# Performance work log

Hardware: AMD Instinct MI355X
Metric: run time of the kernel (lower is better)

## Reference

```python
import jax, jax.numpy as jnp
import numpy as np

# token_type_vocab constants (closed over; original passes a dict)
WORD_TOKEN, SMILES_TOKEN, VALUE_TOKEN, CLS_TOKEN, SEP_TOKEN, MASK_TOKEN = 0, 1, 2, 3, 4, 5
FP_DIM, HID, COL_VOCAB, MAX_POS, TT_VOCAB = 768, 768, 1000, 512, 8
B, S = 64, 512


def setup_inputs() -> dict:
    key = jax.random.key(0)
    ks = jax.random.split(key, 16)
    scale = 0.02
    return {
        "batch_size": B,
        "max_batch_seq_len": S,
        "SMILES_fps": jax.random.normal(ks[0], (B, S, FP_DIM), jnp.float32),
        "word_tokens_ref": jax.random.randint(ks[1], (B, S), 0, COL_VOCAB),
        "values_ref": jax.random.normal(ks[2], (B, S), jnp.float32),
        "token_type_ids": jax.random.randint(ks[3], (B, S), 0, 6),
        "position_ids": jax.random.randint(ks[4], (B, S), 0, MAX_POS),
        "fc1_w": jax.random.normal(ks[5], (FP_DIM, 4 * FP_DIM), jnp.float32) * scale,
        "fc1_b": jnp.zeros((4 * FP_DIM,), jnp.float32),
        "fc2_w": jax.random.normal(ks[6], (4 * FP_DIM, HID), jnp.float32) * scale,
        "fc2_b": jnp.zeros((HID,), jnp.float32),
        "prop_emb": jax.random.normal(ks[7], (COL_VOCAB, HID), jnp.float32) * scale,
        "val_w": jax.random.normal(ks[8], (HID,), jnp.float32) * scale,  # Linear(1, HID) weight
        "val_b": jnp.zeros((HID,), jnp.float32),
        "pos_emb": jax.random.normal(ks[9], (MAX_POS, HID), jnp.float32) * scale,
        "type_emb": jax.random.normal(ks[10], (TT_VOCAB, HID), jnp.float32) * scale,
        "ln_g": jnp.ones((HID,), jnp.float32),
        "ln_b": jnp.zeros((HID,), jnp.float32),
    }


def reference(batch_size, max_batch_seq_len, SMILES_fps, word_tokens_ref, values_ref,
              token_type_ids, position_ids, fc1_w, fc1_b, fc2_w, fc2_b, prop_emb,
              val_w, val_b, pos_emb, type_emb, ln_g, ln_b):
    word_mask = token_type_ids == WORD_TOKEN
    smiles_mask = token_type_ids == SMILES_TOKEN
    value_mask = token_type_ids == VALUE_TOKEN
    # Faithful to source: '&' of mutually exclusive equalities -> always False
    special_mask = (token_type_ids == CLS_TOKEN) & (token_type_ids == SEP_TOKEN) & (token_type_ids == MASK_TOKEN)

    # branch embeddings computed densely, selected per token (masks are disjoint)
    word_e = prop_emb[word_tokens_ref]                                   # [B,S,H]
    smiles_e = jax.nn.relu(jnp.einsum('bsf,fd->bsd', SMILES_fps, fc1_w) + fc1_b)
    smiles_e = jnp.einsum('bsf,fd->bsd', smiles_e, fc2_w) + fc2_b        # [B,S,H]
    value_e = values_ref[..., None] * val_w + val_b                      # [B,S,H]
    special_e = type_emb[token_type_ids]                                 # [B,S,H]

    input_embeddings = jnp.zeros_like(word_e)
    input_embeddings = jnp.where(word_mask[..., None], word_e, input_embeddings)
    input_embeddings = jnp.where(smiles_mask[..., None], smiles_e, input_embeddings)
    input_embeddings = jnp.where(value_mask[..., None], value_e, input_embeddings)
    input_embeddings = jnp.where(special_mask[..., None], special_e, input_embeddings)

    emb = input_embeddings + pos_emb[position_ids] + type_emb[token_type_ids]
    mu = jnp.mean(emb, axis=-1, keepdims=True)
    var = jnp.mean(jnp.square(emb - mu), axis=-1, keepdims=True)
    emb = (emb - mu) * jax.lax.rsqrt(var + 1e-12) * ln_g + ln_b
    return emb  # dropout_rate=0 (eval): identity
```

## Files before the change

### kernel.cpp

```cpp
#include <hip/hip_runtime.h>
#include <hip/hip_bf16.h>
#include <stdint.h>


typedef __bf16 bf16x8 __attribute__((ext_vector_type(8)));
typedef float f32x4 __attribute__((ext_vector_type(4)));

__device__ __forceinline__ unsigned short f2bf(float f) {
  union { float f; unsigned int u; } c; c.f = f;
  unsigned int u = c.u;
  return (unsigned short)((u + 0x7FFFu + ((u >> 16) & 1u)) >> 16);
}
__device__ __forceinline__ float bf2f(unsigned short b) {
  union { unsigned int u; float f; } c; c.u = ((unsigned int)b) << 16;
  return c.f;
}
__device__ __forceinline__ unsigned pk2(float a, float b) {
  return (unsigned)f2bf(a) | ((unsigned)f2bf(b) << 16);
}
__device__ __forceinline__ void barrier_sync() {
  asm volatile("" ::: "memory");
  __builtin_amdgcn_sched_barrier(0);
  __builtin_amdgcn_s_barrier();
  __builtin_amdgcn_sched_barrier(0);
  asm volatile("" ::: "memory");
}

__global__ __launch_bounds__(256) void k_prep(
    const float* __restrict__ fc1_w, const float* __restrict__ fc2_w,
    unsigned short* __restrict__ w1t, unsigned short* __restrict__ w2t,
    int* __restrict__ counter) {
  if (blockIdx.x == 0 && threadIdx.x == 0) *counter = 0;
  __shared__ float tile[32][33];
  int b = blockIdx.x;
  const float* src;
  unsigned short* dst;
  int R, C, bx, by;
  if (b < 2304) {
    src = fc1_w; dst = w1t; R = 768; C = 3072;
    bx = (b % 96) * 32; by = (b / 96) * 32;
  } else {
    b -= 2304;
    src = fc2_w; dst = w2t; R = 3072; C = 768;
    bx = (b % 24) * 32; by = (b / 24) * 32;
  }
  int tx = threadIdx.x & 31;
  int ty = threadIdx.x >> 5;
#pragma unroll
  for (int i = 0; i < 4; i++) {
    int r = by + ty + i * 8;
    tile[ty + i * 8][tx] = src[(size_t)r * C + bx + tx];
  }
  __syncthreads();
#pragma unroll
  for (int i = 0; i < 4; i++) {
    int c = bx + ty + i * 8;
    dst[(size_t)c * R + by + tx] = f2bf(tile[tx][ty + i * 8]);
  }
}

__global__ void k_compact(const int* __restrict__ tt, int* __restrict__ counter,
                          int* __restrict__ idx, int* __restrict__ slot, int BS) {
  int t = blockIdx.x * 256 + threadIdx.x;
  if (t >= BS) return;
  if (tt[t] == 1) {
    int s = atomicAdd(counter, 1);
    idx[s] = t;
    slot[t] = s;
  }
}

__global__ __launch_bounds__(256) void k_gemm1(
    const float* __restrict__ fps, const int* __restrict__ idx,
    const unsigned short* __restrict__ BT,
    const float* __restrict__ bias,
    unsigned short* __restrict__ C,
    const int* __restrict__ counter, int cap) {
  int n = *counter;
  int n_pad = (n + 127) & ~127;
  if (n_pad > cap) n_pad = cap;
  const int mb = n_pad >> 7;

  const int bid = blockIdx.x;
  const int xcd = bid & 7;
  const int j = bid >> 3;
  const int mc = xcd >> 1, cc = xcd & 1;
  const int q = mb >> 2, r = mb & 3;
  const int mlen = q + (mc < r ? 1 : 0);
  const int mbase = mc * q + (mc < r ? mc : r);
  if (j >= mlen * 12) return;
  const int m_blk = mbase + j / 12;
  const int nb = cc * 12 + j % 12;
  const int m0 = m_blk * 128, n0 = nb * 128;

  __shared__ __attribute__((aligned(128))) char smem[65536];
  auto lds = (__attribute__((address_space(3))) char*)smem;
  const int t = threadIdx.x;
  const int wave = t >> 6, lane = t & 63;
  const int wm = (wave >> 1) * 64, wn = (wave & 1) * 64;

  const float* arow[4];
  bool avalid[4];
#pragma unroll
  for (int i = 0; i < 4; i++) {
    int c = i * 256 + t;
    int rr = c >> 3;
    int koff = ((c & 7) ^ (rr & 7)) << 3;
    int grow = m0 + rr;
    avalid[i] = grow < n;
    arow[i] = fps + (size_t)(avalid[i] ? idx[grow] : 0) * 768 + koff;
  }

  f32x4 acc[4][4] = {};
  float4 av[4][2];

  auto loadA = [&](int kt) {
#pragma unroll
    for (int i = 0; i < 4; i++) {
      if (avalid[i]) {
        const float4* p = (const float4*)(arow[i] + kt * 64);
        av[i][0] = p[0];
        av[i][1] = p[1];
      } else {
        av[i][0] = make_float4(0.f, 0.f, 0.f, 0.f);
        av[i][1] = make_float4(0.f, 0.f, 0.f, 0.f);
      }
    }
  };
  auto stageB = [&](int kt, int bufbase) {
#pragma unroll
    for (int i = 0; i < 4; i++) {
      int c = i * 256 + t;
      int rr = c >> 3;
      const unsigned short* gb =
          BT + (size_t)(n0 + rr) * 768 + kt * 64 + (((c & 7) ^ (rr & 7)) << 3);
      __builtin_amdgcn_global_load_lds(
          (const __attribute__((address_space(1))) void*)gb,
          (__attribute__((address_space(3))) void*)(lds + bufbase + 16384 +
                                                    i * 4096 + wave * 1024),
          16, 0, 0);
    }
  };
  auto writeA = [&](int bufbase) {
#pragma unroll
    for (int i = 0; i < 4; i++) {
      int c = i * 256 + t;
      uint4 w;
      w.x = pk2(av[i][0].x, av[i][0].y);
      w.y = pk2(av[i][0].z, av[i][0].w);
      w.z = pk2(av[i][1].x, av[i][1].y);
      w.w = pk2(av[i][1].z, av[i][1].w);
      *(uint4*)(smem + bufbase + c * 16) = w;
    }
  };
  auto compute = [&](int bufbase) {
#pragma unroll
    for (int kk = 0; kk < 2; kk++) {
      bf16x8 af[4], bfr[4];
      int kbyte = (kk * 32 + ((lane >> 4) * 8)) * 2;
#pragma unroll
      for (int mi = 0; mi < 4; mi++) {
        int rr = wm + mi * 16 + (lane & 15);
        af[mi] = *(const bf16x8*)(smem + bufbase + rr * 128 + (kbyte ^ ((rr & 7) << 4)));
      }
#pragma unroll
      for (int ni = 0; ni < 4; ni++) {
        int rr = wn + ni * 16 + (lane & 15);
        bfr[ni] = *(const bf16x8*)(smem + bufbase + 16384 + rr * 128 + (kbyte ^ ((rr & 7) << 4)));
      }
#pragma unroll
      for (int mi = 0; mi < 4; mi++)
#pragma unroll
        for (int ni = 0; ni < 4; ni++)
          acc[mi][ni] = __builtin_amdgcn_mfma_f32_16x16x32_bf16(
              af[mi], bfr[ni], acc[mi][ni], 0, 0, 0);
    }
  };

  loadA(0);
  stageB(0, 0);
  writeA(0);
  asm volatile("s_waitcnt lgkmcnt(0)" ::: "memory");

  for (int it = 0; it < 12; ++it) {
    const int cur = it & 1, nxt = cur ^ 1;
    if (it + 1 < 12) {
      loadA(it + 1);
      stageB(it + 1, nxt * 32768);
      __builtin_amdgcn_sched_barrier(0);
      asm volatile("s_waitcnt vmcnt(12)" ::: "memory");
    } else {
      asm volatile("s_waitcnt vmcnt(0)" ::: "memory");
    }
    barrier_sync();
    compute(cur * 32768);
    if (it + 1 < 12) writeA(nxt * 32768);
    asm volatile("s_waitcnt lgkmcnt(0)" ::: "memory");
    barrier_sync();
  }

#pragma unroll
  for (int ni = 0; ni < 4; ni++) {
    int col = n0 + wn + ni * 16 + (lane & 15);
    float bv = bias[col];
#pragma unroll
    for (int mi = 0; mi < 4; mi++) {
#pragma unroll
      for (int j2 = 0; j2 < 4; j2++) {
        int row = m0 + wm + mi * 16 + ((lane >> 4) * 4) + j2;
        float v = acc[mi][ni][j2] + bv;
        v = v > 0.f ? v : 0.f;
        C[(size_t)row * 3072 + col] = f2bf(v);
      }
    }
  }
}

template <int NB, int KS>
__global__ __launch_bounds__(256) void k_gemm2(
    const unsigned short* __restrict__ A,
    const unsigned short* __restrict__ BT,
    unsigned short* __restrict__ C,
    const int* __restrict__ counter, int cap) {
  int n = *counter;
  int n_pad = (n + 127) & ~127;
  if (n_pad > cap) n_pad = cap;
  const int mb = n_pad >> 7;

  constexpr int NCOL = NB * KS;
  constexpr int C_CH = (KS == 4) ? 4 : 2;
  constexpr int A_CH = 8 / C_CH;
  constexpr int CLEN = NCOL / C_CH;

  const int bid = blockIdx.x;
  const int xcd = bid & 7;
  const int j = bid >> 3;
  const int mc = xcd / C_CH, cc = xcd % C_CH;
  const int q = mb / A_CH, r = mb % A_CH;
  const int mlen = q + (mc < r ? 1 : 0);
  const int mbase = mc * q + (mc < r ? mc : r);
  if (j >= mlen * CLEN) return;
  const int m_blk = mbase + j / CLEN;
  const int c_blk = cc * CLEN + j % CLEN;
  const int ks = c_blk / NB;
  const int nb = c_blk % NB;
  const int m0 = m_blk * 128, n0 = nb * 128;
  const int k0g = ks * 768;

  __shared__ __attribute__((aligned(128))) char smem[65536];
  auto lds = (__attribute__((address_space(3))) char*)smem;
  const int t = threadIdx.x;
  const int wave = t >> 6, lane = t & 63;
  const int wm = (wave >> 1) * 64, wn = (wave & 1) * 64;

  f32x4 acc[4][4] = {};

  auto stage = [&](int kt, int bufbase) {
#pragma unroll
    for (int i = 0; i < 4; i++) {
      int c = i * 256 + t;
      int rr = c >> 3;
      int k8 = ((c & 7) ^ (rr & 7)) << 3;
      const unsigned short* ga = A + (size_t)(m0 + rr) * 3072 + k0g + kt * 64 + k8;
      __builtin_amdgcn_global_load_lds(
          (const __attribute__((address_space(1))) void*)ga,
          (__attribute__((address_space(3))) void*)(lds + bufbase + i * 4096 + wave * 1024),
          16, 0, 0);
    }
#pragma unroll
    for (int i = 0; i < 4; i++) {
      int c = i * 256 + t;
      int rr = c >> 3;
      int k8 = ((c & 7) ^ (rr & 7)) << 3;
      const unsigned short* gb = BT + (size_t)(n0 + rr) * 3072 + k0g + kt * 64 + k8;
      __builtin_amdgcn_global_load_lds(
          (const __attribute__((address_space(1))) void*)gb,
          (__attribute__((address_space(3))) void*)(lds + bufbase + 16384 + i * 4096 + wave * 1024),
          16, 0, 0);
    }
  };

  stage(0, 0);
  for (int it = 0; it < 12; ++it) {
    const int cur = it & 1, nxt = cur ^ 1;
    if (it + 1 < 12) {
      stage(it + 1, nxt * 32768);
      __builtin_amdgcn_sched_barrier(0);
      asm volatile("s_waitcnt vmcnt(8)" ::: "memory");
    } else {
      asm volatile("s_waitcnt vmcnt(0)" ::: "memory");
    }
    barrier_sync();
#pragma unroll
    for (int kk = 0; kk < 2; kk++) {
      bf16x8 af[4], bfr[4];
      int kbyte = (kk * 32 + ((lane >> 4) * 8)) * 2;
      const int bufbase = cur * 32768;
#pragma unroll
      for (int mi = 0; mi < 4; mi++) {
        int rr = wm + mi * 16 + (lane & 15);
        af[mi] = *(const bf16x8*)(smem + bufbase + rr * 128 + (kbyte ^ ((rr & 7) << 4)));
      }
#pragma unroll
      for (int ni = 0; ni < 4; ni++) {
        int rr = wn + ni * 16 + (lane & 15);
        bfr[ni] = *(const bf16x8*)(smem + bufbase + 16384 + rr * 128 + (kbyte ^ ((rr & 7) << 4)));
      }
#pragma unroll
      for (int mi = 0; mi < 4; mi++)
#pragma unroll
        for (int ni = 0; ni < 4; ni++)
          acc[mi][ni] = __builtin_amdgcn_mfma_f32_16x16x32_bf16(
              af[mi], bfr[ni], acc[mi][ni], 0, 0, 0);
    }
    asm volatile("s_waitcnt lgkmcnt(0)" ::: "memory");
    barrier_sync();
  }

#pragma unroll
  for (int ni = 0; ni < 4; ni++) {
    int col = n0 + wn + ni * 16 + (lane & 15);
#pragma unroll
    for (int mi = 0; mi < 4; mi++) {
#pragma unroll
      for (int j2 = 0; j2 < 4; j2++) {
        int row = m0 + wm + mi * 16 + ((lane >> 4) * 4) + j2;
        C[((size_t)ks * cap + row) * 768 + col] = f2bf(acc[mi][ni][j2]);
      }
    }
  }
}

template <int KS>
__global__ __launch_bounds__(256) void k_assemble(
    const unsigned short* __restrict__ sout, const float* __restrict__ fc2b,
    const int* __restrict__ slot,
    const int* __restrict__ ttid, const int* __restrict__ word,
    const float* __restrict__ values, const int* __restrict__ posid,
    const float* __restrict__ prop, const float* __restrict__ valw,
    const float* __restrict__ valb, const float* __restrict__ pose,
    const float* __restrict__ tye, const float* __restrict__ lng,
    const float* __restrict__ lnb, float* __restrict__ out, int BS, int cap) {
  int wave = threadIdx.x >> 6, lane = threadIdx.x & 63;
  int t = blockIdx.x * 4 + wave;
  if (t >= BS) return;
  int tt = ttid[t];

  float v[12];
  if (tt == 1) {
    int sl = slot[t];
    const ushort4* pr[KS];
#pragma unroll
    for (int p = 0; p < KS; p++)
      pr[p] = (const ushort4*)(sout + ((size_t)p * cap + sl) * 768);
    const float4* b4 = (const float4*)fc2b;
#pragma unroll
    for (int i = 0; i < 3; i++) {
      float4 b = b4[lane + (i << 6)];
      float a0 = b.x, a1 = b.y, a2 = b.z, a3 = b.w;
#pragma unroll
      for (int p = 0; p < KS; p++) {
        ushort4 u = pr[p][lane + (i << 6)];
        a0 += bf2f(u.x); a1 += bf2f(u.y); a2 += bf2f(u.z); a3 += bf2f(u.w);
      }
      v[4 * i] = a0; v[4 * i + 1] = a1; v[4 * i + 2] = a2; v[4 * i + 3] = a3;
    }
  } else if (tt == 0) {
    const float4* row = (const float4*)(prop + (size_t)word[t] * 768);
#pragma unroll
    for (int i = 0; i < 3; i++) {
      float4 x = row[lane + (i << 6)];
      v[4 * i] = x.x; v[4 * i + 1] = x.y; v[4 * i + 2] = x.z; v[4 * i + 3] = x.w;
    }
  } else if (tt == 2) {
    float val = values[t];
#pragma unroll
    for (int i = 0; i < 3; i++) {
      float4 w = ((const float4*)valw)[lane + (i << 6)];
      float4 b = ((const float4*)valb)[lane + (i << 6)];
      v[4 * i] = val * w.x + b.x; v[4 * i + 1] = val * w.y + b.y;
      v[4 * i + 2] = val * w.z + b.z; v[4 * i + 3] = val * w.w + b.w;
    }
  } else {
#pragma unroll
    for (int j = 0; j < 12; j++) v[j] = 0.f;
  }

  const float4* p4 = (const float4*)(pose + (size_t)posid[t] * 768);
  const float4* ty4 = (const float4*)(tye + (size_t)tt * 768);
#pragma unroll
  for (int i = 0; i < 3; i++) {
    float4 p = p4[lane + (i << 6)];
    float4 y = ty4[lane + (i << 6)];
    v[4 * i] += p.x + y.x; v[4 * i + 1] += p.y + y.y;
    v[4 * i + 2] += p.z + y.z; v[4 * i + 3] += p.w + y.w;
  }

  float s = 0.f;
#pragma unroll
  for (int j = 0; j < 12; j++) s += v[j];
#pragma unroll
  for (int o = 32; o >= 1; o >>= 1) s += __shfl_xor(s, o);
  float mu = s * (1.0f / 768.0f);

  float qv = 0.f;
#pragma unroll
  for (int j = 0; j < 12; j++) { float d = v[j] - mu; qv += d * d; }
#pragma unroll
  for (int o = 32; o >= 1; o >>= 1) qv += __shfl_xor(qv, o);
  float rs = 1.0f / sqrtf(qv * (1.0f / 768.0f) + 1e-12f);

  float4* o4 = (float4*)(out + (size_t)t * 768);
#pragma unroll
  for (int i = 0; i < 3; i++) {
    float4 g = ((const float4*)lng)[lane + (i << 6)];
    float4 b = ((const float4*)lnb)[lane + (i << 6)];
    float4 r;
    r.x = (v[4 * i] - mu) * rs * g.x + b.x;
    r.y = (v[4 * i + 1] - mu) * rs * g.y + b.y;
    r.z = (v[4 * i + 2] - mu) * rs * g.z + b.z;
    r.w = (v[4 * i + 3] - mu) * rs * g.w + b.w;
    o4[lane + (i << 6)] = r;
  }
}

extern "C" void kernel_launch(void* const* d_in, const int* in_sizes, int n_in,
                              void* d_out, int out_size, void* d_ws, size_t ws_size,
                              hipStream_t stream) {
  const int BS = in_sizes[3];
  const float* fps    = (const float*)d_in[2];
  const int*   word   = (const int*)d_in[3];
  const float* values = (const float*)d_in[4];
  const int*   tt     = (const int*)d_in[5];
  const int*   pos    = (const int*)d_in[6];
  const float* fc1_w  = (const float*)d_in[7];
  const float* fc1_b  = (const float*)d_in[8];
  const float* fc2_w  = (const float*)d_in[9];
  const float* fc2_b  = (const float*)d_in[10];
  const float* prop   = (const float*)d_in[11];
  const float* valw   = (const float*)d_in[12];
  const float* valb   = (const float*)d_in[13];
  const float* pose   = (const float*)d_in[14];
  const float* tye    = (const float*)d_in[15];
  const float* lng    = (const float*)d_in[16];
  const float* lnb    = (const float*)d_in[17];
  float* out = (float*)d_out;

  char* ws = (char*)d_ws;
  const size_t off_idx  = 256;
  const size_t off_slot = off_idx + (size_t)BS * 4;
  const size_t off_w1t  = off_slot + (size_t)BS * 4;
  const size_t off_w2t  = off_w1t + (size_t)768 * 3072 * 2;
  const size_t off_h1   = off_w2t + (size_t)3072 * 768 * 2;
  const size_t fixed    = off_h1;
  size_t avail = ws_size > fixed ? ws_size - fixed : 0;

  const size_t per_tok4 = 3072 * 2 + 4 * 768 * 2;
  const bool splitk = avail >= (size_t)8192 * per_tok4;

  int cap;
  if (splitk) {
    cap = 8192;
  } else {
    const size_t per_tok1 = 3072 * 2 + 768 * 2;
    long c = (long)(avail / per_tok1);
    c &= ~511L;
    if (c > BS) c = BS;
    if (c < 512) c = 512;
    cap = (int)c;
  }
  const int MBcap = cap / 128;

  const size_t off_sout = off_h1 + (size_t)cap * 3072 * 2;

  int* counter = (int*)(ws + 0);
  int* idx     = (int*)(ws + off_idx);
  int* slot    = (int*)(ws + off_slot);
  unsigned short* w1t = (unsigned short*)(ws + off_w1t);
  unsigned short* w2t = (unsigned short*)(ws + off_w2t);
  unsigned short* h1  = (unsigned short*)(ws + off_h1);
  unsigned short* sout = (unsigned short*)(ws + off_sout);

  k_prep<<<4608, 256, 0, stream>>>(fc1_w, fc2_w, w1t, w2t, counter);
  k_compact<<<(BS + 255) / 256, 256, 0, stream>>>(tt, counter, idx, slot, BS);

  k_gemm1<<<24 * MBcap, 256, 0, stream>>>(fps, idx, w1t, fc1_b, h1, counter, cap);

  if (splitk) {
    k_gemm2<6, 4><<<24 * MBcap, 256, 0, stream>>>(h1, w2t, sout, counter, cap);
    k_assemble<4><<<(BS + 3) / 4, 256, 0, stream>>>(
        sout, fc2_b, slot, tt, word, values, pos, prop, valw, valb, pose, tye,
        lng, lnb, out, BS, cap);
  } else {
    k_gemm2<6, 1><<<6 * MBcap, 256, 0, stream>>>(h1, w2t, sout, counter, cap);
    k_assemble<1><<<(BS + 3) / 4, 256, 0, stream>>>(
        sout, fc2_b, slot, tt, word, values, pos, prop, valw, valb, pose, tye,
        lng, lnb, out, BS, cap);
  }
}
```

Before: 139.0 us.

## Pre-gather bf16 SMILES rows and overlap non-SMILES assembly with GEMM2

Gathers and converts the selected SMILES fp rows to bf16 in a separate pass fused into the weight-transpose kernel. GEMM1 can then stage both operands with direct global-to-LDS loads instead of register loads and in-kernel conversion. Non-SMILES token assembly and LayerNorm now run as extra blocks inside the GEMM2 launch, and a smaller kernel finalises only the SMILES tokens. This removes the slot array and trades an extra bf16 activation buffer and an extra pass over the gathered rows for a shorter GEMM1 inner loop and overlap of independent work.

```diff
diff --git a/kernel.cpp b/kernel.cpp
--- a/kernel.cpp
+++ b/kernel.cpp
@@ -14,9 +14,6 @@
 __device__ __forceinline__ float bf2f(unsigned short b) {
   union { unsigned int u; float f; } c; c.u = ((unsigned int)b) << 16;
   return c.f;
-}
-__device__ __forceinline__ unsigned pk2(float a, float b) {
-  return (unsigned)f2bf(a) | ((unsigned)f2bf(b) << 16);
 }
 __device__ __forceinline__ void barrier_sync() {
   asm volatile("" ::: "memory");
@@ -26,13 +23,77 @@
   asm volatile("" ::: "memory");
 }
 
-__global__ __launch_bounds__(256) void k_prep(
+__device__ __forceinline__ void ln_store(float v[12], const float* __restrict__ lng,
+                                         const float* __restrict__ lnb,
+                                         float* __restrict__ out, int t, int lane) {
+  float s = 0.f;
+#pragma unroll
+  for (int j = 0; j < 12; j++) s += v[j];
+#pragma unroll
+  for (int o = 32; o >= 1; o >>= 1) s += __shfl_xor(s, o);
+  float mu = s * (1.0f / 768.0f);
+  float qv = 0.f;
+#pragma unroll
+  for (int j = 0; j < 12; j++) { float d = v[j] - mu; qv += d * d; }
+#pragma unroll
+  for (int o = 32; o >= 1; o >>= 1) qv += __shfl_xor(qv, o);
+  float rs = 1.0f / sqrtf(qv * (1.0f / 768.0f) + 1e-12f);
+  float4* o4 = (float4*)(out + (size_t)t * 768);
+#pragma unroll
+  for (int i = 0; i < 3; i++) {
+    float4 g = ((const float4*)lng)[lane + (i << 6)];
+    float4 b = ((const float4*)lnb)[lane + (i << 6)];
+    float4 r;
+    r.x = (v[4 * i] - mu) * rs * g.x + b.x;
+    r.y = (v[4 * i + 1] - mu) * rs * g.y + b.y;
+    r.z = (v[4 * i + 2] - mu) * rs * g.z + b.z;
+    r.w = (v[4 * i + 3] - mu) * rs * g.w + b.w;
+    o4[lane + (i << 6)] = r;
+  }
+}
+
+__global__ void k_compact(const int* __restrict__ tt, int* __restrict__ counter,
+                          int* __restrict__ idx, int BS) {
+  int t = blockIdx.x * 256 + threadIdx.x;
+  if (t >= BS) return;
+  if (tt[t] == 1) {
+    int s = atomicAdd(counter, 1);
+    idx[s] = t;
+  }
+}
+
+__global__ __launch_bounds__(256) void k_prepg(
     const float* __restrict__ fc1_w, const float* __restrict__ fc2_w,
+    const float* __restrict__ fps, const int* __restrict__ idx,
+    const int* __restrict__ counter,
     unsigned short* __restrict__ w1t, unsigned short* __restrict__ w2t,
-    int* __restrict__ counter) {
-  if (blockIdx.x == 0 && threadIdx.x == 0) *counter = 0;
+    unsigned short* __restrict__ A1, int cap) {
+  int b = blockIdx.x;
+  if (b >= 4608) {
+    int wave = threadIdx.x >> 6, lane = threadIdx.x & 63;
+    int s = (b - 4608) * 4 + wave;
+    int n = *counter;
+    int n_pad = (n + 127) & ~127;
+    if (n_pad > cap) n_pad = cap;
+    if (s >= n_pad) return;
+    ushort4* dst = (ushort4*)(A1 + (size_t)s * 768);
+    if (s < n) {
+      const float4* srcr = (const float4*)(fps + (size_t)idx[s] * 768);
+#pragma unroll
+      for (int i = 0; i < 3; i++) {
+        float4 v = srcr[lane + (i << 6)];
+        ushort4 o;
+        o.x = f2bf(v.x); o.y = f2bf(v.y); o.z = f2bf(v.z); o.w = f2bf(v.w);
+        dst[lane + (i << 6)] = o;
+      }
+    } else {
+      ushort4 z = {0, 0, 0, 0};
+#pragma unroll
+      for (int i = 0; i < 3; i++) dst[lane + (i << 6)] = z;
+    }
+    return;
+  }
   __shared__ float tile[32][33];
-  int b = blockIdx.x;
   const float* src;
   unsigned short* dst;
   int R, C, bx, by;
@@ -59,22 +120,9 @@
   }
 }
 
-__global__ void k_compact(const int* __restrict__ tt, int* __restrict__ counter,
-                          int* __restrict__ idx, int* __restrict__ slot, int BS) {
-  int t = blockIdx.x * 256 + threadIdx.x;
-  if (t >= BS) return;
-  if (tt[t] == 1) {
-    int s = atomicAdd(counter, 1);
-    idx[s] = t;
-    slot[t] = s;
-  }
-}
-
 __global__ __launch_bounds__(256) void k_gemm1(
-    const float* __restrict__ fps, const int* __restrict__ idx,
-    const unsigned short* __restrict__ BT,
-    const float* __restrict__ bias,
-    unsigned short* __restrict__ C,
+    const unsigned short* __restrict__ A, const unsigned short* __restrict__ BT,
+    const float* __restrict__ bias, unsigned short* __restrict__ C,
     const int* __restrict__ counter, int cap) {
   int n = *counter;
   int n_pad = (n + 127) & ~127;
@@ -89,9 +137,8 @@
   const int mlen = q + (mc < r ? 1 : 0);
   const int mbase = mc * q + (mc < r ? mc : r);
   if (j >= mlen * 12) return;
-  const int m_blk = mbase + j / 12;
-  const int nb = cc * 12 + j % 12;
-  const int m0 = m_blk * 128, n0 = nb * 128;
+  const int m0 = (mbase + j / 12) * 128;
+  const int n0 = (cc * 12 + j % 12) * 128;
 
   __shared__ __attribute__((aligned(128))) char smem[65536];
   auto lds = (__attribute__((address_space(3))) char*)smem;
@@ -99,61 +146,45 @@
   const int wave = t >> 6, lane = t & 63;
   const int wm = (wave >> 1) * 64, wn = (wave & 1) * 64;
 
-  const float* arow[4];
-  bool avalid[4];
-#pragma unroll
-  for (int i = 0; i < 4; i++) {
-    int c = i * 256 + t;
-    int rr = c >> 3;
-    int koff = ((c & 7) ^ (rr & 7)) << 3;
-    int grow = m0 + rr;
-    avalid[i] = grow < n;
-    arow[i] = fps + (size_t)(avalid[i] ? idx[grow] : 0) * 768 + koff;
-  }
-
   f32x4 acc[4][4] = {};
-  float4 av[4][2];
-
-  auto loadA = [&](int kt) {
-#pragma unroll
-    for (int i = 0; i < 4; i++) {
-      if (avalid[i]) {
-        const float4* p = (const float4*)(arow[i] + kt * 64);
-        av[i][0] = p[0];
-        av[i][1] = p[1];
-      } else {
-        av[i][0] = make_float4(0.f, 0.f, 0.f, 0.f);
-        av[i][1] = make_float4(0.f, 0.f, 0.f, 0.f);
-      }
-    }
-  };
-  auto stageB = [&](int kt, int bufbase) {
+
+  auto stage = [&](int kt, int bufbase) {
 #pragma unroll
     for (int i = 0; i < 4; i++) {
       int c = i * 256 + t;
       int rr = c >> 3;
-      const unsigned short* gb =
-          BT + (size_t)(n0 + rr) * 768 + kt * 64 + (((c & 7) ^ (rr & 7)) << 3);
+      int k8 = ((c & 7) ^ (rr & 7)) << 3;
+      const unsigned short* ga = A + (size_t)(m0 + rr) * 768 + kt * 64 + k8;
+      __builtin_amdgcn_global_load_lds(
+          (const __attribute__((address_space(1))) void*)ga,
+          (__attribute__((address_space(3))) void*)(lds + bufbase + i * 4096 + wave * 1024),
+          16, 0, 0);
+    }
+#pragma unroll
+    for (int i = 0; i < 4; i++) {
+      int c = i * 256 + t;
+      int rr = c >> 3;
+      int k8 = ((c & 7) ^ (rr & 7)) << 3;
+      const unsigned short* gb = BT + (size_t)(n0 + rr) * 768 + kt * 64 + k8;
       __builtin_amdgcn_global_load_lds(
           (const __attribute__((address_space(1))) void*)gb,
-          (__attribute__((address_space(3))) void*)(lds + bufbase + 16384 +
-                                                    i * 4096 + wave * 1024),
+          (__attribute__((address_space(3))) void*)(lds + bufbase + 16384 + i * 4096 + wave * 1024),
           16, 0, 0);
     }
   };
-  auto writeA = [&](int bufbase) {
-#pragma unroll
-    for (int i = 0; i < 4; i++) {
-      int c = i * 256 + t;
-      uint4 w;
-      w.x = pk2(av[i][0].x, av[i][0].y);
-      w.y = pk2(av[i][0].z, av[i][0].w);
-      w.z = pk2(av[i][1].x, av[i][1].y);
-      w.w = pk2(av[i][1].z, av[i][1].w);
-      *(uint4*)(smem + bufbase + c * 16) = w;
-    }
-  };
-  auto compute = [&](int bufbase) {
+
+  stage(0, 0);
+  for (int it = 0; it < 12; ++it) {
+    const int cur = it & 1, nxt = cur ^ 1;
+    if (it + 1 < 12) {
+      stage(it + 1, nxt * 32768);
+      __builtin_amdgcn_sched_barrier(0);
+      asm volatile("s_waitcnt vmcnt(8)" ::: "memory");
+    } else {
+      asm volatile("s_waitcnt vmcnt(0)" ::: "memory");
+    }
+    barrier_sync();
+    const int bufbase = cur * 32768;
 #pragma unroll
     for (int kk = 0; kk < 2; kk++) {
       bf16x8 af[4], bfr[4];
@@ -175,26 +206,6 @@
           acc[mi][ni] = __builtin_amdgcn_mfma_f32_16x16x32_bf16(
               af[mi], bfr[ni], acc[mi][ni], 0, 0, 0);
     }
-  };
-
-  loadA(0);
-  stageB(0, 0);
-  writeA(0);
-  asm volatile("s_waitcnt lgkmcnt(0)" ::: "memory");
-
-  for (int it = 0; it < 12; ++it) {
-    const int cur = it & 1, nxt = cur ^ 1;
-    if (it + 1 < 12) {
-      loadA(it + 1);
-      stageB(it + 1, nxt * 32768);
-      __builtin_amdgcn_sched_barrier(0);
-      asm volatile("s_waitcnt vmcnt(12)" ::: "memory");
-    } else {
-      asm volatile("s_waitcnt vmcnt(0)" ::: "memory");
-    }
-    barrier_sync();
-    compute(cur * 32768);
-    if (it + 1 < 12) writeA(nxt * 32768);
     asm volatile("s_waitcnt lgkmcnt(0)" ::: "memory");
     barrier_sync();
   }
@@ -216,41 +227,82 @@
   }
 }
 
-template <int NB, int KS>
-__global__ __launch_bounds__(256) void k_gemm2(
+__global__ __launch_bounds__(256) void k_gemm2f(
     const unsigned short* __restrict__ A,
     const unsigned short* __restrict__ BT,
     unsigned short* __restrict__ C,
-    const int* __restrict__ counter, int cap) {
+    const int* __restrict__ counter, int cap, int NGEMM, int NASM,
+    const int* __restrict__ ttid, const int* __restrict__ word,
+    const float* __restrict__ values, const int* __restrict__ posid,
+    const float* __restrict__ prop, const float* __restrict__ valw,
+    const float* __restrict__ valb, const float* __restrict__ pose,
+    const float* __restrict__ tye, const float* __restrict__ lng,
+    const float* __restrict__ lnb, float* __restrict__ out, int BS) {
+  const int bid = blockIdx.x;
+  const int t = threadIdx.x;
+  const int wave = t >> 6, lane = t & 63;
+
+  if (bid >= NGEMM) {
+    int ab = bid - NGEMM;
+    for (int tok = ab * 4 + wave; tok < BS; tok += NASM * 4) {
+      int tt = ttid[tok];
+      if (tt == 1) continue;
+      float v[12];
+      if (tt == 0) {
+        const float4* row = (const float4*)(prop + (size_t)word[tok] * 768);
+#pragma unroll
+        for (int i = 0; i < 3; i++) {
+          float4 x = row[lane + (i << 6)];
+          v[4 * i] = x.x; v[4 * i + 1] = x.y; v[4 * i + 2] = x.z; v[4 * i + 3] = x.w;
+        }
+      } else if (tt == 2) {
+        float val = values[tok];
+#pragma unroll
+        for (int i = 0; i < 3; i++) {
+          float4 w = ((const float4*)valw)[lane + (i << 6)];
+          float4 b = ((const float4*)valb)[lane + (i << 6)];
+          v[4 * i] = val * w.x + b.x; v[4 * i + 1] = val * w.y + b.y;
+          v[4 * i + 2] = val * w.z + b.z; v[4 * i + 3] = val * w.w + b.w;
+        }
+      } else {
+#pragma unroll
+        for (int j = 0; j < 12; j++) v[j] = 0.f;
+      }
+      const float4* p4 = (const float4*)(pose + (size_t)posid[tok] * 768);
+      const float4* ty4 = (const float4*)(tye + (size_t)tt * 768);
+#pragma unroll
+      for (int i = 0; i < 3; i++) {
+        float4 p = p4[lane + (i << 6)];
+        float4 y = ty4[lane + (i << 6)];
+        v[4 * i] += p.x + y.x; v[4 * i + 1] += p.y + y.y;
+        v[4 * i + 2] += p.z + y.z; v[4 * i + 3] += p.w + y.w;
+      }
+      ln_store(v, lng, lnb, out, tok, lane);
+    }
+    return;
+  }
+
   int n = *counter;
   int n_pad = (n + 127) & ~127;
   if (n_pad > cap) n_pad = cap;
   const int mb = n_pad >> 7;
 
-  constexpr int NCOL = NB * KS;
-  constexpr int C_CH = (KS == 4) ? 4 : 2;
-  constexpr int A_CH = 8 / C_CH;
-  constexpr int CLEN = NCOL / C_CH;
-
-  const int bid = blockIdx.x;
   const int xcd = bid & 7;
   const int j = bid >> 3;
-  const int mc = xcd / C_CH, cc = xcd % C_CH;
-  const int q = mb / A_CH, r = mb % A_CH;
+  const int mc = xcd >> 2, cc = xcd & 3;
+  const int q = mb >> 1, r = mb & 1;
   const int mlen = q + (mc < r ? 1 : 0);
   const int mbase = mc * q + (mc < r ? mc : r);
-  if (j >= mlen * CLEN) return;
-  const int m_blk = mbase + j / CLEN;
-  const int c_blk = cc * CLEN + j % CLEN;
-  const int ks = c_blk / NB;
-  const int nb = c_blk % NB;
+  if (j >= mlen * 6) return;
+  const int m_blk = mbase + j / 6;
+  const int c_blk = cc * 6 + j % 6;
+  const int ks = c_blk / 6;
+  const int nb = c_blk % 6;
   const int m0 = m_blk * 128, n0 = nb * 128;
   const int k0g = ks * 768;
 
   __shared__ __attribute__((aligned(128))) char smem[65536];
   auto lds = (__attribute__((address_space(3))) char*)smem;
-  const int t = threadIdx.x;
-  const int wave = t >> 6, lane = t & 63;
   const int wm = (wave >> 1) * 64, wn = (wave & 1) * 64;
 
   f32x4 acc[4][4] = {};
@@ -291,11 +343,11 @@
       asm volatile("s_waitcnt vmcnt(0)" ::: "memory");
     }
     barrier_sync();
+    const int bufbase = cur * 32768;
 #pragma unroll
     for (int kk = 0; kk < 2; kk++) {
       bf16x8 af[4], bfr[4];
       int kbyte = (kk * 32 + ((lane >> 4) * 8)) * 2;
-      const int bufbase = cur * 32768;
 #pragma unroll
       for (int mi = 0; mi < 4; mi++) {
         int rr = wm + mi * 16 + (lane & 15);
@@ -331,63 +383,38 @@
   }
 }
 
-template <int KS>
-__global__ __launch_bounds__(256) void k_assemble(
+__global__ __launch_bounds__(256) void k_asm_s(
     const unsigned short* __restrict__ sout, const float* __restrict__ fc2b,
-    const int* __restrict__ slot,
-    const int* __restrict__ ttid, const int* __restrict__ word,
-    const float* __restrict__ values, const int* __restrict__ posid,
-    const float* __restrict__ prop, const float* __restrict__ valw,
-    const float* __restrict__ valb, const float* __restrict__ pose,
+    const int* __restrict__ idx, const int* __restrict__ counter,
+    const int* __restrict__ posid, const float* __restrict__ pose,
     const float* __restrict__ tye, const float* __restrict__ lng,
-    const float* __restrict__ lnb, float* __restrict__ out, int BS, int cap) {
+    const float* __restrict__ lnb, float* __restrict__ out, int cap) {
   int wave = threadIdx.x >> 6, lane = threadIdx.x & 63;
-  int t = blockIdx.x * 4 + wave;
-  if (t >= BS) return;
-  int tt = ttid[t];
+  int s = blockIdx.x * 4 + wave;
+  int n = *counter;
+  if (n > cap) n = cap;
+  if (s >= n) return;
+  int tok = idx[s];
 
   float v[12];
-  if (tt == 1) {
-    int sl = slot[t];
-    const ushort4* pr[KS];
-#pragma unroll
-    for (int p = 0; p < KS; p++)
-      pr[p] = (const ushort4*)(sout + ((size_t)p * cap + sl) * 768);
-    const float4* b4 = (const float4*)fc2b;
-#pragma unroll
-    for (int i = 0; i < 3; i++) {
-      float4 b = b4[lane + (i << 6)];
-      float a0 = b.x, a1 = b.y, a2 = b.z, a3 = b.w;
-#pragma unroll
-      for (int p = 0; p < KS; p++) {
-        ushort4 u = pr[p][lane + (i << 6)];
-        a0 += bf2f(u.x); a1 += bf2f(u.y); a2 += bf2f(u.z); a3 += bf2f(u.w);
-      }
-      v[4 * i] = a0; v[4 * i + 1] = a1; v[4 * i + 2] = a2; v[4 * i + 3] = a3;
-    }
-  } else if (tt == 0) {
-    const float4* row = (const float4*)(prop + (size_t)word[t] * 768);
-#pragma unroll
-    for (int i = 0; i < 3; i++) {
-      float4 x = row[lane + (i << 6)];
-      v[4 * i] = x.x; v[4 * i + 1] = x.y; v[4 * i + 2] = x.z; v[4 * i + 3] = x.w;
-    }
-  } else if (tt == 2) {
-    float val = values[t];
-#pragma unroll
-    for (int i = 0; i < 3; i++) {
-      float4 w = ((const float4*)valw)[lane + (i << 6)];
-      float4 b = ((const float4*)valb)[lane + (i << 6)];
-      v[4 * i] = val * w.x + b.x; v[4 * i + 1] = val * w.y + b.y;
-      v[4 * i + 2] = val * w.z + b.z; v[4 * i + 3] = val * w.w + b.w;
-    }
-  } else {
-#pragma unroll
-    for (int j = 0; j < 12; j++) v[j] = 0.f;
-  }
-
-  const float4* p4 = (const float4*)(pose + (size_t)posid[t] * 768);
-  const float4* ty4 = (const float4*)(tye + (size_t)tt * 768);
+  const ushort4* pr[4];
+#pragma unroll
+  for (int p = 0; p < 4; p++)
+    pr[p] = (const ushort4*)(sout + ((size_t)p * cap + s) * 768);
+  const float4* b4 = (const float4*)fc2b;
+#pragma unroll
+  for (int i = 0; i < 3; i++) {
+    float4 b = b4[lane + (i << 6)];
+    float a0 = b.x, a1 = b.y, a2 = b.z, a3 = b.w;
+#pragma unroll
+    for (int p = 0; p < 4; p++) {
+      ushort4 u = pr[p][lane + (i << 6)];
+      a0 += bf2f(u.x); a1 += bf2f(u.y); a2 += bf2f(u.z); a3 += bf2f(u.w);
+    }
+    v[4 * i] = a0; v[4 * i + 1] = a1; v[4 * i + 2] = a2; v[4 * i + 3] = a3;
+  }
+  const float4* p4 = (const float4*)(pose + (size_t)posid[tok] * 768);
+  const float4* ty4 = (const float4*)(tye + (size_t)1 * 768);
 #pragma unroll
   for (int i = 0; i < 3; i++) {
     float4 p = p4[lane + (i << 6)];
@@ -395,33 +422,7 @@
     v[4 * i] += p.x + y.x; v[4 * i + 1] += p.y + y.y;
     v[4 * i + 2] += p.z + y.z; v[4 * i + 3] += p.w + y.w;
   }
-
-  float s = 0.f;
-#pragma unroll
-  for (int j = 0; j < 12; j++) s += v[j];
-#pragma unroll
-  for (int o = 32; o >= 1; o >>= 1) s += __shfl_xor(s, o);
-  float mu = s * (1.0f / 768.0f);
-
-  float qv = 0.f;
-#pragma unroll
-  for (int j = 0; j < 12; j++) { float d = v[j] - mu; qv += d * d; }
-#pragma unroll
-  for (int o = 32; o >= 1; o >>= 1) qv += __shfl_xor(qv, o);
-  float rs = 1.0f / sqrtf(qv * (1.0f / 768.0f) + 1e-12f);
-
-  float4* o4 = (float4*)(out + (size_t)t * 768);
-#pragma unroll
-  for (int i = 0; i < 3; i++) {
-    float4 g = ((const float4*)lng)[lane + (i << 6)];
-    float4 b = ((const float4*)lnb)[lane + (i << 6)];
-    float4 r;
-    r.x = (v[4 * i] - mu) * rs * g.x + b.x;
-    r.y = (v[4 * i + 1] - mu) * rs * g.y + b.y;
-    r.z = (v[4 * i + 2] - mu) * rs * g.z + b.z;
-    r.w = (v[4 * i + 3] - mu) * rs * g.w + b.w;
-    o4[lane + (i << 6)] = r;
-  }
+  ln_store(v, lng, lnb, out, tok, lane);
 }
 
 extern "C" void kernel_launch(void* const* d_in, const int* in_sizes, int n_in,
@@ -448,53 +449,47 @@
 
   char* ws = (char*)d_ws;
   const size_t off_idx  = 256;
-  const size_t off_slot = off_idx + (size_t)BS * 4;
-  const size_t off_w1t  = off_slot + (size_t)BS * 4;
+  const size_t off_w1t  = off_idx + (size_t)BS * 4;
   const size_t off_w2t  = off_w1t + (size_t)768 * 3072 * 2;
-  const size_t off_h1   = off_w2t + (size_t)3072 * 768 * 2;
-  const size_t fixed    = off_h1;
+  const size_t off_A1   = off_w2t + (size_t)3072 * 768 * 2;
+  const size_t fixed    = off_A1;
   size_t avail = ws_size > fixed ? ws_size - fixed : 0;
 
-  const size_t per_tok4 = 3072 * 2 + 4 * 768 * 2;
-  const bool splitk = avail >= (size_t)8192 * per_tok4;
-
-  int cap;
-  if (splitk) {
-    cap = 8192;
-  } else {
-    const size_t per_tok1 = 3072 * 2 + 768 * 2;
-    long c = (long)(avail / per_tok1);
-    c &= ~511L;
-    if (c > BS) c = BS;
-    if (c < 512) c = 512;
+  const size_t per_tok4 = 768 * 2 + 3072 * 2 + 4 * 768 * 2;
+  int cap = 8192;
+  if (avail < (size_t)8192 * per_tok4) {
+    long c = (long)(avail / per_tok4);
+    c &= ~127L;
+    if (c < 128) c = 128;
     cap = (int)c;
   }
   const int MBcap = cap / 128;
 
+  const size_t off_h1   = off_A1 + (size_t)cap * 768 * 2;
   const size_t off_sout = off_h1 + (size_t)cap * 3072 * 2;
 
   int* counter = (int*)(ws + 0);
   int* idx     = (int*)(ws + off_idx);
-  int* slot    = (int*)(ws + off_slot);
   unsigned short* w1t = (unsigned short*)(ws + off_w1t);
   unsigned short* w2t = (unsigned short*)(ws + off_w2t);
+  unsigned short* A1  = (unsigned short*)(ws + off_A1);
   unsigned short* h1  = (unsigned short*)(ws + off_h1);
   unsigned short* sout = (unsigned short*)(ws + off_sout);
 
-  k_prep<<<4608, 256, 0, stream>>>(fc1_w, fc2_w, w1t, w2t, counter);
-  k_compact<<<(BS + 255) / 256, 256, 0, stream>>>(tt, counter, idx, slot, BS);
-
-  k_gemm1<<<24 * MBcap, 256, 0, stream>>>(fps, idx, w1t, fc1_b, h1, counter, cap);
-
-  if (splitk) {
-    k_gemm2<6, 4><<<24 * MBcap, 256, 0, stream>>>(h1, w2t, sout, counter, cap);
-    k_assemble<4><<<(BS + 3) / 4, 256, 0, stream>>>(
-        sout, fc2_b, slot, tt, word, values, pos, prop, valw, valb, pose, tye,
-        lng, lnb, out, BS, cap);
-  } else {
-    k_gemm2<6, 1><<<6 * MBcap, 256, 0, stream>>>(h1, w2t, sout, counter, cap);
-    k_assemble<1><<<(BS + 3) / 4, 256, 0, stream>>>(
-        sout, fc2_b, slot, tt, word, values, pos, prop, valw, valb, pose, tye,
-        lng, lnb, out, BS, cap);
-  }
-}
+  hipMemsetAsync(counter, 0, 4, stream);
+  k_compact<<<(BS + 255) / 256, 256, 0, stream>>>(tt, counter, idx, BS);
+
+  k_prepg<<<4608 + cap / 4, 256, 0, stream>>>(
+      fc1_w, fc2_w, fps, idx, counter, w1t, w2t, A1, cap);
+
+  k_gemm1<<<24 * MBcap, 256, 0, stream>>>(A1, w1t, fc1_b, h1, counter, cap);
+
+  const int NGEMM = 24 * MBcap;
+  const int NASM = 1024;
+  k_gemm2f<<<NGEMM + NASM, 256, 0, stream>>>(
+      h1, w2t, sout, counter, cap, NGEMM, NASM,
+      tt, word, values, pos, prop, valw, valb, pose, tye, lng, lnb, out, BS);
+
+  k_asm_s<<<cap / 4, 256, 0, stream>>>(
+      sout, fc2_b, idx, counter, pos, pose, tye, lng, lnb, out, cap);
+}
```

After: 134.7 us. 3.1% less time.
